# Kernel optimization log

Hardware: AMD Instinct MI355X
Metric: run time of the kernel (lower is better)

## Reference

```python
import jax, jax.numpy as jnp
import numpy as np

B, T, C = 2, 2048, 768
NH = 12
HS = C // NH


def setup_inputs() -> dict:
    key = jax.random.key(0)
    k1, k2, k3 = jax.random.split(key, 3)
    x = jax.random.normal(k1, (B, T, C), dtype=jnp.float32)
    # c_attn: Linear(C, 3C). Stored as (C, 3C) so y = x @ w + b (same math as torch x @ W.T + b).
    w_attn = jax.random.normal(k2, (C, 3 * C), dtype=jnp.float32) * (1.0 / np.sqrt(C))
    b_attn = jax.random.normal(k3, (3 * C,), dtype=jnp.float32) * 0.02
    return {"x": x, "w_attn": w_attn, "b_attn": b_attn}


def reference(x, w_attn, b_attn):
    b, t, c = x.shape
    qkv = x @ w_attn + b_attn                      # [B, T, 3C]
    q, k, v = jnp.split(qkv, 3, axis=-1)
    # [B, T, C] -> [B, NH, T, HS]
    q = q.reshape(b, t, NH, HS).transpose(0, 2, 1, 3)
    k = k.reshape(b, t, NH, HS).transpose(0, 2, 1, 3)
    v = v.reshape(b, t, NH, HS).transpose(0, 2, 1, 3)
    scale = 1.0 / np.sqrt(HS).astype(np.float32)
    wei = jnp.einsum("bhqd,bhkd->bhqk", q, k) * scale   # [B, NH, T, T]
    causal = jnp.tril(jnp.ones((t, t), dtype=bool))
    wei = jnp.where(causal[None, None, :, :], wei, -jnp.inf)
    wei = jax.nn.softmax(wei, axis=-1)
    out = jnp.einsum("bhqk,bhkd->bhqd", wei, v)          # [B, NH, T, HS]
    # NOTE: original module returns here, before head-merge / output projection.
    return out
```

## Files before the change

### kernel.cpp

```cpp
#include <hip/hip_runtime.h>

typedef __bf16 bf16_t;
typedef __bf16 bf16x8 __attribute__((ext_vector_type(8)));
typedef __bf16 bf16x4 __attribute__((ext_vector_type(4)));
typedef _Float16 f16x2 __attribute__((ext_vector_type(2)));
typedef _Float16 f16x4 __attribute__((ext_vector_type(4)));
typedef _Float16 f16x8 __attribute__((ext_vector_type(8)));
typedef float f32x4 __attribute__((ext_vector_type(4)));

#define B_   2
#define T_   2048
#define C_   768
#define NH_  12
#define HS_  64
#define N3_  2304
#define M_   4096
#define QSCALE 0.18033688011112042f

__device__ __forceinline__ bf16_t f2bf(float f) {
  unsigned u = __builtin_bit_cast(unsigned, f);
  u += 0x7fffu + ((u >> 16) & 1u);
  unsigned short s = (unsigned short)(u >> 16);
  return __builtin_bit_cast(bf16_t, s);
}

__global__ __launch_bounds__(256) void cvt_xw_kernel(const float* __restrict__ x,
                                                     const float* __restrict__ w,
                                                     bf16_t* __restrict__ xb,
                                                     bf16_t* __restrict__ wt) {
  __shared__ float tile[32][33];
  int bx = blockIdx.x;
  if (bx < 3072) {
    int i = (bx * 256 + threadIdx.x) * 4;
    float4 v = *reinterpret_cast<const float4*>(x + i);
    bf16x4 pk;
    pk[0] = f2bf(v.x);
    pk[1] = f2bf(v.y);
    pk[2] = f2bf(v.z);
    pk[3] = f2bf(v.w);
    *reinterpret_cast<bf16x4*>(xb + i) = pk;
  } else {
    int b = bx - 3072;
    int k0 = (b % 24) * 32, n0 = (b / 24) * 32;
    int tx = threadIdx.x & 31, ty = threadIdx.x >> 5;
#pragma unroll
    for (int i = 0; i < 4; i++)
      tile[ty + i * 8][tx] = w[(size_t)(k0 + ty + i * 8) * N3_ + n0 + tx];
    __syncthreads();
    int n = threadIdx.x >> 3, kq = threadIdx.x & 7;
    bf16x4 pk;
#pragma unroll
    for (int j = 0; j < 4; j++) pk[j] = f2bf(tile[kq * 4 + j][n]);
    *reinterpret_cast<bf16x4*>(wt + (size_t)(n0 + n) * C_ + k0 + kq * 4) = pk;
  }
}

__global__ __launch_bounds__(256) void gemm_qkv(const bf16_t* __restrict__ xb,
                                                const bf16_t* __restrict__ wt,
                                                const float* __restrict__ bias,
                                                bf16_t* __restrict__ qout,
                                                bf16_t* __restrict__ kout,
                                                _Float16* __restrict__ va) {
  __shared__ bf16_t As[2][64 * 32];
  __shared__ bf16_t Bs[2][128 * 32];
  const int tid = threadIdx.x;
  const int lane = tid & 63, wave = tid >> 6;
  const int wm = wave >> 1, wn = wave & 1;
  const int quad = lane >> 4, l15 = lane & 15;

  const int id = (int)blockIdx.x;
  const int xcd = id & 7, r = id >> 3;
  const int cx = r % 9, ry = r / 9;
  const int bx = (xcd & 1) * 9 + cx;
  const int by = (xcd >> 1) * 16 + ry;
  const int row0 = by * 64;
  const int col0 = bx * 128;
  const bool isqk = (col0 < 1536);

  f32x4 acc[2][4];
#pragma unroll
  for (int mi = 0; mi < 2; mi++)
#pragma unroll
    for (int ni = 0; ni < 4; ni++) acc[mi][ni] = f32x4{0.f, 0.f, 0.f, 0.f};

  const int r0 = tid >> 2, q0 = tid & 3;
  const int r1 = (256 + tid) >> 2, q1 = (256 + tid) & 3;
  const bf16_t* gA0 = xb + (size_t)(row0 + r0) * C_ + q0 * 8;
  const bf16_t* gB0 = wt + (size_t)(col0 + r0) * C_ + q0 * 8;
  const bf16_t* gB1 = wt + (size_t)(col0 + r1) * C_ + q1 * 8;
  const int ldsOff0 = (wave * 64) * 16;
  const int ldsOff1 = (256 + wave * 64) * 16;

  auto STAGE = [&](int buf, int k0) {
    __builtin_amdgcn_global_load_lds((const __attribute__((address_space(1))) void*)(gA0 + k0),
                                     (__attribute__((address_space(3))) void*)((char*)As[buf] + ldsOff0), 16, 0, 0);
    __builtin_amdgcn_global_load_lds((const __attribute__((address_space(1))) void*)(gB0 + k0),
                                     (__attribute__((address_space(3))) void*)((char*)Bs[buf] + ldsOff0), 16, 0, 0);
    __builtin_amdgcn_global_load_lds((const __attribute__((address_space(1))) void*)(gB1 + k0),
                                     (__attribute__((address_space(3))) void*)((char*)Bs[buf] + ldsOff1), 16, 0, 0);
  };

  STAGE(0, 0);
  __syncthreads();

  constexpr int NT = C_ / 32;
#pragma unroll 2
  for (int t = 0; t < NT; ++t) {
    const int cur = t & 1;
    if (t + 1 < NT) STAGE(cur ^ 1, (t + 1) * 32);

    bf16x8 af[2], bfr[4];
#pragma unroll
    for (int mi = 0; mi < 2; mi++)
      af[mi] = *reinterpret_cast<const bf16x8*>(&As[cur][(wm * 32 + mi * 16 + l15) * 32 + quad * 8]);
#pragma unroll
    for (int ni = 0; ni < 4; ni++)
      bfr[ni] = *reinterpret_cast<const bf16x8*>(&Bs[cur][(wn * 64 + ni * 16 + l15) * 32 + quad * 8]);
    if (isqk) {
#pragma unroll
      for (int mi = 0; mi < 2; mi++)
#pragma unroll
        for (int ni = 0; ni < 4; ni++)
          acc[mi][ni] = __builtin_amdgcn_mfma_f32_16x16x32_bf16(bfr[ni], af[mi], acc[mi][ni], 0, 0, 0);
    } else {
#pragma unroll
      for (int mi = 0; mi < 2; mi++)
#pragma unroll
        for (int ni = 0; ni < 4; ni++)
          acc[mi][ni] = __builtin_amdgcn_mfma_f32_16x16x32_bf16(af[mi], bfr[ni], acc[mi][ni], 0, 0, 0);
    }
    __syncthreads();
  }

  if (isqk) {
#pragma unroll
    for (int mi = 0; mi < 2; mi++) {
      int t = row0 + wm * 32 + mi * 16 + l15;
      int b = t >> 11, tt = t & 2047;
#pragma unroll
      for (int ni = 0; ni < 4; ni++) {
        int cN0 = col0 + wn * 64 + ni * 16 + quad * 4;
        int which = cN0 / 768;
        int rem = cN0 - which * 768;
        int h = rem >> 6, d0 = rem & 63;
        float4 bv = *reinterpret_cast<const float4*>(bias + cN0);
        float sc = which ? 1.0f : QSCALE;
        bf16x4 pack;
        pack[0] = f2bf((acc[mi][ni][0] + bv.x) * sc);
        pack[1] = f2bf((acc[mi][ni][1] + bv.y) * sc);
        pack[2] = f2bf((acc[mi][ni][2] + bv.z) * sc);
        pack[3] = f2bf((acc[mi][ni][3] + bv.w) * sc);
        bf16_t* dst = which ? kout : qout;
        *reinterpret_cast<bf16x4*>(dst + (((size_t)b * NH_ + h) * T_ + tt) * HS_ + d0) = pack;
      }
    }
  } else {
#pragma unroll
    for (int mi = 0; mi < 2; mi++) {
      int trow = row0 + wm * 32 + mi * 16 + quad * 4;
      int b = trow >> 11, tt = trow & 2047;
      int kt = tt >> 6, nj = (tt >> 4) & 3, qd = (tt >> 2) & 3;
#pragma unroll
      for (int ni = 0; ni < 4; ni++) {
        int cN = col0 + wn * 64 + ni * 16 + l15;
        int rem = cN - 1536;
        int h = rem >> 6, d = rem & 63;
        int bh = b * NH_ + h;
        float bv = bias[cN];
        f16x4 pk;
#pragma unroll
        for (int r2 = 0; r2 < 4; r2++) pk[r2] = (_Float16)(acc[mi][ni][r2] + bv);
        size_t off = ((((((size_t)bh * 32 + kt) * 4 + nj) * 4 + qd) * 16 + (d & 15)) * 16) + (d >> 4) * 4;
        *reinterpret_cast<f16x4*>(va + off) = pk;
      }
    }
  }
}

__global__ __launch_bounds__(128) void attn_kernel(const bf16_t* __restrict__ qb,
                                                   const bf16_t* __restrict__ kb,
                                                   const _Float16* __restrict__ va,
                                                   float* __restrict__ out) {
  __shared__ bf16_t Ks[2][64][72];
  __shared__ _Float16 Vs[2][4][2][64][8];
  const int tid = threadIdx.x;
  const int lane = tid & 63, wave = tid >> 6;
  const int quad = lane >> 4, l15 = lane & 15;
  const int id = (int)blockIdx.x;
  const int xcd = id & 7, within = id >> 3;
  const int bh = xcd * 3 + within / 32;
  const int pairIdx = within & 31;
  const bf16_t* Qg = qb + (size_t)bh * T_ * HS_;
  const bf16_t* Kg = kb + (size_t)bh * T_ * HS_;
  const _Float16* Vg = va + (size_t)bh * 32 * 4096;

  const int krow = tid >> 1, kcolB = (tid & 1) * 64;
  const int vni = tid >> 5, vlane = (tid & 31) * 2;

  int4 rk0, rk1, rk2, rk3, rv0, rv1, rv2, rv3;
  const char* kp;
  const char* vp;
  auto GLOAD = [&]() {
    rk0 = *reinterpret_cast<const int4*>(kp);
    rk1 = *reinterpret_cast<const int4*>(kp + 16);
    rk2 = *reinterpret_cast<const int4*>(kp + 32);
    rk3 = *reinterpret_cast<const int4*>(kp + 48);
    rv0 = *reinterpret_cast<const int4*>(vp);
    rv1 = *reinterpret_cast<const int4*>(vp + 16);
    rv2 = *reinterpret_cast<const int4*>(vp + 32);
    rv3 = *reinterpret_cast<const int4*>(vp + 48);
    kp += 8192; vp += 8192;
  };
  auto SSTORE = [&](int buf) {
    char* kd = (char*)&Ks[buf][krow][0] + kcolB;
    *reinterpret_cast<int4*>(kd) = rk0;
    *reinterpret_cast<int4*>(kd + 16) = rk1;
    *reinterpret_cast<int4*>(kd + 32) = rk2;
    *reinterpret_cast<int4*>(kd + 48) = rk3;
    *reinterpret_cast<int4*>(&Vs[buf][vni][0][vlane][0]) = rv0;
    *reinterpret_cast<int4*>(&Vs[buf][vni][1][vlane][0]) = rv1;
    *reinterpret_cast<int4*>(&Vs[buf][vni][0][vlane + 1][0]) = rv2;
    *reinterpret_cast<int4*>(&Vs[buf][vni][1][vlane + 1][0]) = rv3;
  };

#pragma unroll
  for (int part = 0; part < 2; part++) {
    const int qtile = part ? pairIdx : 63 - pairIdx;
    const int qrow_base = qtile * 32 + wave * 16;
    const int qmax = qrow_base + 15;
    const int qcol = qrow_base + l15;
    const int nkt = (qtile >> 1) + 1;

    bf16x8 bq0 = *reinterpret_cast<const bf16x8*>(Qg + (size_t)qcol * HS_ + quad * 8);
    bf16x8 bq1 = *reinterpret_cast<const bf16x8*>(Qg + (size_t)qcol * HS_ + 32 + quad * 8);

    float lsum = 0.f;
    f32x4 Oacc[4];
#pragma unroll
    for (int mi = 0; mi < 4; mi++) Oacc[mi] = f32x4{0.f, 0.f, 0.f, 0.f};

    kp = (const char*)Kg + krow * 128 + kcolB;
    vp = (const char*)Vg + tid * 64;
    GLOAD();
    __syncthreads();
    SSTORE(0);
    __syncthreads();

    for (int kt = 0; kt < nkt; kt++) {
      const int cur = kt & 1;
      const bool last = (kt + 1 >= nkt);
      if (!last) GLOAD();

      const bool diag = (kt == nkt - 1);
      f16x4 pf[4];
#pragma unroll
      for (int ni = 0; ni < 4; ni++) {
        if (diag && (kt * 64 + ni * 16 > qmax)) continue;
        bf16x8 ka0 = *reinterpret_cast<const bf16x8*>(&Ks[cur][ni * 16 + l15][quad * 8]);
        bf16x8 ka1 = *reinterpret_cast<const bf16x8*>(&Ks[cur][ni * 16 + l15][32 + quad * 8]);
        f32x4 s = {0.f, 0.f, 0.f, 0.f};
        s = __builtin_amdgcn_mfma_f32_16x16x32_bf16(ka0, bq0, s, 0, 0, 0);
        s = __builtin_amdgcn_mfma_f32_16x16x32_bf16(ka1, bq1, s, 0, 0, 0);
        float p0 = __builtin_amdgcn_exp2f(s[0]);
        float p1 = __builtin_amdgcn_exp2f(s[1]);
        float p2 = __builtin_amdgcn_exp2f(s[2]);
        float p3 = __builtin_amdgcn_exp2f(s[3]);
        if (diag) {
          int jb = kt * 64 + ni * 16 + quad * 4;
          if (jb + 0 > qcol) p0 = 0.f;
          if (jb + 1 > qcol) p1 = 0.f;
          if (jb + 2 > qcol) p2 = 0.f;
          if (jb + 3 > qcol) p3 = 0.f;
        }
        lsum += (p0 + p1) + (p2 + p3);
        f16x2 lo2 = __builtin_bit_cast(f16x2, __builtin_amdgcn_cvt_pkrtz(p0, p1));
        f16x2 hi2 = __builtin_bit_cast(f16x2, __builtin_amdgcn_cvt_pkrtz(p2, p3));
        pf[ni] = f16x4{lo2[0], lo2[1], hi2[0], hi2[1]};
      }
#pragma unroll
      for (int ni = 0; ni < 4; ni++) {
        if (diag && (kt * 64 + ni * 16 > qmax)) continue;
#pragma unroll
        for (int p = 0; p < 2; p++) {
          f16x8 vv = *reinterpret_cast<const f16x8*>(&Vs[cur][ni][p][lane][0]);
          f16x4 lo = __builtin_shufflevector(vv, vv, 0, 1, 2, 3);
          f16x4 hi = __builtin_shufflevector(vv, vv, 4, 5, 6, 7);
          Oacc[2 * p]     = __builtin_amdgcn_mfma_f32_16x16x16f16(lo, pf[ni], Oacc[2 * p], 0, 0, 0);
          Oacc[2 * p + 1] = __builtin_amdgcn_mfma_f32_16x16x16f16(hi, pf[ni], Oacc[2 * p + 1], 0, 0, 0);
        }
      }

      if (!last) {
        SSTORE(1 - cur);
        __syncthreads();
      }
    }

    lsum += __shfl_xor(lsum, 16, 64);
    lsum += __shfl_xor(lsum, 32, 64);
    float rinv = 1.0f / lsum;

#pragma unroll
    for (int mi = 0; mi < 4; mi++) {
      float4 o;
      o.x = Oacc[mi][0] * rinv;
      o.y = Oacc[mi][1] * rinv;
      o.z = Oacc[mi][2] * rinv;
      o.w = Oacc[mi][3] * rinv;
      *reinterpret_cast<float4*>(out + ((size_t)bh * T_ + qcol) * HS_ + mi * 16 + quad * 4) = o;
    }
  }
}

extern "C" void kernel_launch(void* const* d_in, const int* in_sizes, int n_in,
                              void* d_out, int out_size, void* d_ws, size_t ws_size,
                              hipStream_t stream) {
  const float* x = (const float*)d_in[0];
  const float* w = (const float*)d_in[1];
  const float* bias = (const float*)d_in[2];
  float* out = (float*)d_out;

  char* ws = (char*)d_ws;
  bf16_t* xb = (bf16_t*)(ws);
  bf16_t* wt = (bf16_t*)(ws + 6291456);
  bf16_t* qb = (bf16_t*)(ws + 6291456 + 3538944);
  bf16_t* kb = qb + 3145728;
  _Float16* va = (_Float16*)(kb + 3145728);

  cvt_xw_kernel<<<dim3(3072 + 1728), dim3(256), 0, stream>>>(x, w, xb, wt);
  gemm_qkv<<<dim3(1152), dim3(256), 0, stream>>>(xb, wt, bias, qb, kb, va);
  attn_kernel<<<dim3(768), dim3(128), 0, stream>>>(qb, kb, va, out);
}
```

Before: 142.1 us.

## Use 4-wave blocks over 64-row query tiles, dropping paired-tile balancing

The attention kernel now uses 256 threads (4 waves) per block, and each block handles one 64-row query tile instead of two paired 32-row tiles. Each K/V tile load from shared memory is reused by twice as many query rows, and staging work per thread is halved. Block order runs from the longest tiles to the shortest (qtile = 31 - r/3), which replaces the explicit long/short pairing that balanced causal work. This risks worse load balance and a tail of short blocks.

```diff
diff --git a/kernel.cpp b/kernel.cpp
--- a/kernel.cpp
+++ b/kernel.cpp
@@ -177,7 +177,7 @@
   }
 }
 
-__global__ __launch_bounds__(128) void attn_kernel(const bf16_t* __restrict__ qb,
+__global__ __launch_bounds__(256) void attn_kernel(const bf16_t* __restrict__ qb,
                                                    const bf16_t* __restrict__ kb,
                                                    const _Float16* __restrict__ va,
                                                    float* __restrict__ out) {
@@ -187,128 +187,115 @@
   const int lane = tid & 63, wave = tid >> 6;
   const int quad = lane >> 4, l15 = lane & 15;
   const int id = (int)blockIdx.x;
-  const int xcd = id & 7, within = id >> 3;
-  const int bh = xcd * 3 + within / 32;
-  const int pairIdx = within & 31;
+  const int xcd = id & 7, r = id >> 3;
+  const int bh = xcd * 3 + (r % 3);
+  const int qtile = 31 - r / 3;
   const bf16_t* Qg = qb + (size_t)bh * T_ * HS_;
   const bf16_t* Kg = kb + (size_t)bh * T_ * HS_;
   const _Float16* Vg = va + (size_t)bh * 32 * 4096;
 
-  const int krow = tid >> 1, kcolB = (tid & 1) * 64;
-  const int vni = tid >> 5, vlane = (tid & 31) * 2;
-
-  int4 rk0, rk1, rk2, rk3, rv0, rv1, rv2, rv3;
+  const int krow = tid >> 2, kcol = (tid & 3) * 16;
+  const int vni = tid >> 6, vlane = tid & 63;
+
+  int4 rk0, rk1, rv0, rv1;
   const char* kp;
   const char* vp;
   auto GLOAD = [&]() {
     rk0 = *reinterpret_cast<const int4*>(kp);
     rk1 = *reinterpret_cast<const int4*>(kp + 16);
-    rk2 = *reinterpret_cast<const int4*>(kp + 32);
-    rk3 = *reinterpret_cast<const int4*>(kp + 48);
     rv0 = *reinterpret_cast<const int4*>(vp);
     rv1 = *reinterpret_cast<const int4*>(vp + 16);
-    rv2 = *reinterpret_cast<const int4*>(vp + 32);
-    rv3 = *reinterpret_cast<const int4*>(vp + 48);
     kp += 8192; vp += 8192;
   };
   auto SSTORE = [&](int buf) {
-    char* kd = (char*)&Ks[buf][krow][0] + kcolB;
+    char* kd = (char*)&Ks[buf][krow][kcol];
     *reinterpret_cast<int4*>(kd) = rk0;
     *reinterpret_cast<int4*>(kd + 16) = rk1;
-    *reinterpret_cast<int4*>(kd + 32) = rk2;
-    *reinterpret_cast<int4*>(kd + 48) = rk3;
     *reinterpret_cast<int4*>(&Vs[buf][vni][0][vlane][0]) = rv0;
     *reinterpret_cast<int4*>(&Vs[buf][vni][1][vlane][0]) = rv1;
-    *reinterpret_cast<int4*>(&Vs[buf][vni][0][vlane + 1][0]) = rv2;
-    *reinterpret_cast<int4*>(&Vs[buf][vni][1][vlane + 1][0]) = rv3;
   };
 
-#pragma unroll
-  for (int part = 0; part < 2; part++) {
-    const int qtile = part ? pairIdx : 63 - pairIdx;
-    const int qrow_base = qtile * 32 + wave * 16;
-    const int qmax = qrow_base + 15;
-    const int qcol = qrow_base + l15;
-    const int nkt = (qtile >> 1) + 1;
-
-    bf16x8 bq0 = *reinterpret_cast<const bf16x8*>(Qg + (size_t)qcol * HS_ + quad * 8);
-    bf16x8 bq1 = *reinterpret_cast<const bf16x8*>(Qg + (size_t)qcol * HS_ + 32 + quad * 8);
-
-    float lsum = 0.f;
-    f32x4 Oacc[4];
-#pragma unroll
-    for (int mi = 0; mi < 4; mi++) Oacc[mi] = f32x4{0.f, 0.f, 0.f, 0.f};
-
-    kp = (const char*)Kg + krow * 128 + kcolB;
-    vp = (const char*)Vg + tid * 64;
-    GLOAD();
-    __syncthreads();
-    SSTORE(0);
-    __syncthreads();
-
-    for (int kt = 0; kt < nkt; kt++) {
-      const int cur = kt & 1;
-      const bool last = (kt + 1 >= nkt);
-      if (!last) GLOAD();
-
-      const bool diag = (kt == nkt - 1);
-      f16x4 pf[4];
-#pragma unroll
-      for (int ni = 0; ni < 4; ni++) {
-        if (diag && (kt * 64 + ni * 16 > qmax)) continue;
-        bf16x8 ka0 = *reinterpret_cast<const bf16x8*>(&Ks[cur][ni * 16 + l15][quad * 8]);
-        bf16x8 ka1 = *reinterpret_cast<const bf16x8*>(&Ks[cur][ni * 16 + l15][32 + quad * 8]);
-        f32x4 s = {0.f, 0.f, 0.f, 0.f};
-        s = __builtin_amdgcn_mfma_f32_16x16x32_bf16(ka0, bq0, s, 0, 0, 0);
-        s = __builtin_amdgcn_mfma_f32_16x16x32_bf16(ka1, bq1, s, 0, 0, 0);
-        float p0 = __builtin_amdgcn_exp2f(s[0]);
-        float p1 = __builtin_amdgcn_exp2f(s[1]);
-        float p2 = __builtin_amdgcn_exp2f(s[2]);
-        float p3 = __builtin_amdgcn_exp2f(s[3]);
-        if (diag) {
-          int jb = kt * 64 + ni * 16 + quad * 4;
-          if (jb + 0 > qcol) p0 = 0.f;
-          if (jb + 1 > qcol) p1 = 0.f;
-          if (jb + 2 > qcol) p2 = 0.f;
-          if (jb + 3 > qcol) p3 = 0.f;
-        }
-        lsum += (p0 + p1) + (p2 + p3);
-        f16x2 lo2 = __builtin_bit_cast(f16x2, __builtin_amdgcn_cvt_pkrtz(p0, p1));
-        f16x2 hi2 = __builtin_bit_cast(f16x2, __builtin_amdgcn_cvt_pkrtz(p2, p3));
-        pf[ni] = f16x4{lo2[0], lo2[1], hi2[0], hi2[1]};
+  const int qrow_base = qtile * 64 + wave * 16;
+  const int qmax = qrow_base + 15;
+  const int qcol = qrow_base + l15;
+  const int nkt = qtile + 1;
+
+  bf16x8 bq0 = *reinterpret_cast<const bf16x8*>(Qg + (size_t)qcol * HS_ + quad * 8);
+  bf16x8 bq1 = *reinterpret_cast<const bf16x8*>(Qg + (size_t)qcol * HS_ + 32 + quad * 8);
+
+  float lsum = 0.f;
+  f32x4 Oacc[4];
+#pragma unroll
+  for (int mi = 0; mi < 4; mi++) Oacc[mi] = f32x4{0.f, 0.f, 0.f, 0.f};
+
+  kp = (const char*)Kg + krow * 128 + kcol * 2;
+  vp = (const char*)Vg + tid * 32;
+  GLOAD();
+  SSTORE(0);
+  __syncthreads();
+
+  for (int kt = 0; kt < nkt; kt++) {
+    const int cur = kt & 1;
+    const bool last = (kt + 1 >= nkt);
+    if (!last) GLOAD();
+
+    const bool diag = (kt == nkt - 1);
+    f16x4 pf[4];
+#pragma unroll
+    for (int ni = 0; ni < 4; ni++) {
+      if (diag && (kt * 64 + ni * 16 > qmax)) continue;
+      bf16x8 ka0 = *reinterpret_cast<const bf16x8*>(&Ks[cur][ni * 16 + l15][quad * 8]);
+      bf16x8 ka1 = *reinterpret_cast<const bf16x8*>(&Ks[cur][ni * 16 + l15][32 + quad * 8]);
+      f32x4 s = {0.f, 0.f, 0.f, 0.f};
+      s = __builtin_amdgcn_mfma_f32_16x16x32_bf16(ka0, bq0, s, 0, 0, 0);
+      s = __builtin_amdgcn_mfma_f32_16x16x32_bf16(ka1, bq1, s, 0, 0, 0);
+      float p0 = __builtin_amdgcn_exp2f(s[0]);
+      float p1 = __builtin_amdgcn_exp2f(s[1]);
+      float p2 = __builtin_amdgcn_exp2f(s[2]);
+      float p3 = __builtin_amdgcn_exp2f(s[3]);
+      if (diag) {
+        int jb = kt * 64 + ni * 16 + quad * 4;
+        if (jb + 0 > qcol) p0 = 0.f;
+        if (jb + 1 > qcol) p1 = 0.f;
+        if (jb + 2 > qcol) p2 = 0.f;
+        if (jb + 3 > qcol) p3 = 0.f;
       }
-#pragma unroll
-      for (int ni = 0; ni < 4; ni++) {
-        if (diag && (kt * 64 + ni * 16 > qmax)) continue;
-#pragma unroll
-        for (int p = 0; p < 2; p++) {
-          f16x8 vv = *reinterpret_cast<const f16x8*>(&Vs[cur][ni][p][lane][0]);
-          f16x4 lo = __builtin_shufflevector(vv, vv, 0, 1, 2, 3);
-          f16x4 hi = __builtin_shufflevector(vv, vv, 4, 5, 6, 7);
-          Oacc[2 * p]     = __builtin_amdgcn_mfma_f32_16x16x16f16(lo, pf[ni], Oacc[2 * p], 0, 0, 0);
-          Oacc[2 * p + 1] = __builtin_amdgcn_mfma_f32_16x16x16f16(hi, pf[ni], Oacc[2 * p + 1], 0, 0, 0);
-        }
+      lsum += (p0 + p1) + (p2 + p3);
+      f16x2 lo2 = __builtin_bit_cast(f16x2, __builtin_amdgcn_cvt_pkrtz(p0, p1));
+      f16x2 hi2 = __builtin_bit_cast(f16x2, __builtin_amdgcn_cvt_pkrtz(p2, p3));
+      pf[ni] = f16x4{lo2[0], lo2[1], hi2[0], hi2[1]};
+    }
+#pragma unroll
+    for (int ni = 0; ni < 4; ni++) {
+      if (diag && (kt * 64 + ni * 16 > qmax)) continue;
+#pragma unroll
+      for (int p = 0; p < 2; p++) {
+        f16x8 vv = *reinterpret_cast<const f16x8*>(&Vs[cur][ni][p][lane][0]);
+        f16x4 lo = __builtin_shufflevector(vv, vv, 0, 1, 2, 3);
+        f16x4 hi = __builtin_shufflevector(vv, vv, 4, 5, 6, 7);
+        Oacc[2 * p]     = __builtin_amdgcn_mfma_f32_16x16x16f16(lo, pf[ni], Oacc[2 * p], 0, 0, 0);
+        Oacc[2 * p + 1] = __builtin_amdgcn_mfma_f32_16x16x16f16(hi, pf[ni], Oacc[2 * p + 1], 0, 0, 0);
       }
-
-      if (!last) {
-        SSTORE(1 - cur);
-        __syncthreads();
-      }
-    }
-
-    lsum += __shfl_xor(lsum, 16, 64);
-    lsum += __shfl_xor(lsum, 32, 64);
-    float rinv = 1.0f / lsum;
-
-#pragma unroll
-    for (int mi = 0; mi < 4; mi++) {
-      float4 o;
-      o.x = Oacc[mi][0] * rinv;
-      o.y = Oacc[mi][1] * rinv;
-      o.z = Oacc[mi][2] * rinv;
-      o.w = Oacc[mi][3] * rinv;
-      *reinterpret_cast<float4*>(out + ((size_t)bh * T_ + qcol) * HS_ + mi * 16 + quad * 4) = o;
-    }
+    }
+
+    if (!last) {
+      SSTORE(1 - cur);
+      __syncthreads();
+    }
+  }
+
+  lsum += __shfl_xor(lsum, 16, 64);
+  lsum += __shfl_xor(lsum, 32, 64);
+  float rinv = 1.0f / lsum;
+
+#pragma unroll
+  for (int mi = 0; mi < 4; mi++) {
+    float4 o;
+    o.x = Oacc[mi][0] * rinv;
+    o.y = Oacc[mi][1] * rinv;
+    o.z = Oacc[mi][2] * rinv;
+    o.w = Oacc[mi][3] * rinv;
+    *reinterpret_cast<float4*>(out + ((size_t)bh * T_ + qcol) * HS_ + mi * 16 + quad * 4) = o;
   }
 }
 
@@ -329,5 +316,5 @@
 
   cvt_xw_kernel<<<dim3(3072 + 1728), dim3(256), 0, stream>>>(x, w, xb, wt);
   gemm_qkv<<<dim3(1152), dim3(256), 0, stream>>>(xb, wt, bias, qb, kb, va);
-  attn_kernel<<<dim3(768), dim3(128), 0, stream>>>(qb, kb, va, out);
-}
+  attn_kernel<<<dim3(768), dim3(256), 0, stream>>>(qb, kb, va, out);
+}
```

New measurement: 154.4 us. 8.6% more time.
